# Optimization experiments

Hardware: AMD Instinct MI355X
Metric: run time of the kernel (lower is better)

## Reference

```python
import jax, jax.numpy as jnp
import numpy as np

LOG_2PI = float(np.log(2.0 * np.pi))


def setup_inputs() -> dict:
    key = jax.random.key(0)
    k1, k2, k3 = jax.random.split(key, 3)
    N, D, K = 2_000_000, 16, 32
    data = jax.random.normal(k1, (N, D), dtype=jnp.float32)
    means = jax.random.uniform(k2, (K, D), dtype=jnp.float32)  # torch.rand init
    # torch init is eye expanded per component; perturb slightly so the
    # Cholesky / solve paths are exercised with non-trivial values while
    # A @ A.T stays well-conditioned PD.
    cov_parts = (jnp.eye(D, dtype=jnp.float32)[None, :, :]
                 + 0.1 * jax.random.normal(k3, (K, D, D), dtype=jnp.float32))
    log_weights = jnp.zeros((K,), dtype=jnp.float32)
    return {"data": data, "means": means, "cov_parts": cov_parts,
            "log_weights": log_weights}


def _mixture_loglik(data, means, cov_parts, log_weights):
    D = data.shape[-1]
    # covariance_k = A_k @ A_k^T  -> Cholesky factor L_k (lower)
    cov = jnp.einsum('kij,klj->kil', cov_parts, cov_parts)      # [K, D, D]
    chol = jnp.linalg.cholesky(cov)                             # [K, D, D]

    def comp_logprob(mu, L):
        # MVN log_prob for one component over all N points
        diff = data - mu                                        # [N, D]
        # solve L z = diff^T  -> z: [D, N]
        z = jax.scipy.linalg.solve_triangular(L, diff.T, lower=True)
        quad = jnp.sum(z * z, axis=0)                           # [N]
        logdet = jnp.sum(jnp.log(jnp.diagonal(L)))              # 0.5*logdet(cov)
        return -0.5 * (quad + D * LOG_2PI) - logdet             # [N]

    # [N, K] log-likelihood per point per component
    log_liks = jax.vmap(comp_logprob, in_axes=(0, 0), out_axes=1)(means, chol)
    weighted = log_liks + log_weights ** 2                      # note: squared, per source
    return jnp.mean(jax.nn.logsumexp(weighted, axis=1))


def reference(data, means, cov_parts, log_weights):
    return _mixture_loglik(data, means, cov_parts, log_weights)
```

## Files before the change

### kernel.cpp

```cpp
#include <hip/hip_runtime.h>
#include <math.h>


#define LOG_2PI 1.8378770664093453f
#define INV_LN2 1.4426950408889634f
#define LN2_D   0.6931471805599453

typedef float    float4v __attribute__((ext_vector_type(4)));
typedef float    f32x16  __attribute__((ext_vector_type(16)));
typedef _Float16 f16x8   __attribute__((ext_vector_type(8)));
typedef _Float16 f16x2   __attribute__((ext_vector_type(2)));

union H8 { f16x8 h8; f16x2 h2[4]; };

#if __has_builtin(__builtin_amdgcn_exp2f)
#define EXP2F(x) __builtin_amdgcn_exp2f(x)
#else
#define EXP2F(x) exp2f(x)
#endif
#if __has_builtin(__builtin_amdgcn_logf)
#define LOG2F(x) __builtin_amdgcn_logf(x)
#else
#define LOG2F(x) log2f(x)
#endif

static __device__ __forceinline__ f16x2 pk2(float a, float b) {
#if __has_builtin(__builtin_amdgcn_cvt_pkrtz)
  return __builtin_bit_cast(f16x2, __builtin_amdgcn_cvt_pkrtz(a, b));
#else
  f16x2 r; r[0] = (_Float16)a; r[1] = (_Float16)b; return r;
#endif
}

static __device__ __forceinline__ float partner32(float x, bool lo) {
#if __has_builtin(__builtin_amdgcn_permlane32_swap)
  typedef unsigned u32x2 __attribute__((ext_vector_type(2)));
  unsigned u = __builtin_bit_cast(unsigned, x);
  u32x2 r = __builtin_amdgcn_permlane32_swap(u, u, false, false);
  return __builtin_bit_cast(float, lo ? r[1] : r[0]);
#else
  return __shfl_xor(x, 32, 64);
#endif
}

static __device__ __forceinline__ f16x2 sel2(bool c, f16x2 a, f16x2 b) {
  unsigned ua = __builtin_bit_cast(unsigned, a);
  unsigned ub = __builtin_bit_cast(unsigned, b);
  return __builtin_bit_cast(f16x2, c ? ua : ub);
}

__global__ void setup_kernel(const float* __restrict__ means,
                             const float* __restrict__ cov_parts,
                             const float* __restrict__ log_weights,
                             _Float16* __restrict__ W,
                             unsigned* __restrict__ counter)
{
  const int k = blockIdx.x;
  const int i = threadIdx.x;

  if (k == 0 && i == 0) counter[0] = 0u;

  __shared__ float sA[16][17];
  __shared__ float sC[16][17];
  __shared__ float sMu[16];
  __shared__ float sR[16];

  if (i < 16) {
    #pragma unroll
    for (int j = 0; j < 16; ++j) sA[i][j] = cov_parts[(k*16 + i)*16 + j];
    sMu[i] = means[k*16 + i];
  }
  __syncthreads();

  if (i < 16) {
    #pragma unroll
    for (int j = 0; j < 16; ++j) {
      float acc = 0.f;
      #pragma unroll
      for (int l = 0; l < 16; ++l) acc += sA[i][l] * sA[j][l];
      sC[i][j] = acc;
    }
  }
  __syncthreads();

  for (int j = 0; j < 16; ++j) {
    if (i == j) {
      float d = sC[j][j];
      for (int l = 0; l < j; ++l) d -= sC[j][l]*sC[j][l];
      sC[j][j] = sqrtf(d);
    }
    __syncthreads();
    if (i < 16 && i > j) {
      float a = sC[i][j];
      for (int l = 0; l < j; ++l) a -= sC[i][l]*sC[j][l];
      sC[i][j] = a / sC[j][j];
    }
    __syncthreads();
  }

  if (i < 16) {
    float y[16];
    #pragma unroll
    for (int r = 0; r < 16; ++r) {
      float a = (r == i) ? 1.f : 0.f;
      #pragma unroll
      for (int l = 0; l < r; ++l) a -= sC[r][l] * y[l];
      y[r] = a / sC[r][r];
    }
    #pragma unroll
    for (int r = 0; r < 16; ++r) sA[r][i] = y[r];
  }
  __syncthreads();

  if (i < 16) {
    float p[16];
    #pragma unroll
    for (int j = 0; j < 16; ++j) {
      float acc = 0.f;
      #pragma unroll
      for (int l = 0; l < 16; ++l) acc += sA[l][i] * sA[l][j];
      p[j] = acc;
    }
    float ri = 0.f;
    #pragma unroll
    for (int j = 0; j < 16; ++j) ri += p[j] * sMu[j];
    sR[i] = ri;

    #pragma unroll
    for (int j = 0; j < 16; ++j) {
      W[(size_t)(i*64 + (k + 32*(j >> 3)))*8 + (j & 7)] =
          (_Float16)(-0.5f * INV_LN2 * p[j]);
    }
    W[(size_t)(16*64 + (k + 32*(i >> 3)))*8 + (i & 7)] =
        (_Float16)(INV_LN2 * ri);
  }
  __syncthreads();

  if (i == 0) {
    float logdet = 0.f;
    #pragma unroll
    for (int j = 0; j < 16; ++j) logdet += __logf(sC[j][j]);
    float mupmu = 0.f;
    #pragma unroll
    for (int j = 0; j < 16; ++j) mupmu += sMu[j] * sR[j];
    float lw = log_weights[k];
    float c2v = INV_LN2 * (-0.5f*(mupmu + 16.f*LOG_2PI) - logdet + lw*lw);
    #pragma unroll
    for (int v = 0; v < 8; ++v) {
      W[(size_t)(17*64 + k)*8 + v]      = (v == 0) ? (_Float16)c2v : (_Float16)0.f;
      W[(size_t)(17*64 + k + 32)*8 + v] = (_Float16)0.f;
    }
  }
}

__global__ __launch_bounds__(256, 3) void main_kernel(
    const float* __restrict__ data,
    const _Float16* __restrict__ W,
    float* __restrict__ partials,
    unsigned* __restrict__ counter,
    float* __restrict__ out,
    double scale,
    int ntiles)
{
  const int lane = threadIdx.x & 63;
  const int n32  = lane & 31;
  const bool lo  = lane < 32;
  const int gwave  = (int)((blockIdx.x * blockDim.x + threadIdx.x) >> 6);
  const int nwaves = (int)((gridDim.x * blockDim.x) >> 6);

  f16x8 Wf[18];
  #pragma unroll
  for (int c = 0; c < 18; ++c)
    Wf[c] = *(const f16x8*)(W + (size_t)(c*64 + lane)*8);

  H8 bC;
  #pragma unroll
  for (int j = 0; j < 4; ++j) bC.h2[j] = pk2(0.f, 0.f);
  if (lo) bC.h2[0] = pk2(1.f, 0.f);

  float accsum = 0.f;

  const char* ptrA = (const char*)data + ((size_t)gwave*2048 + (size_t)n32*64);
  const char* ptrB = ptrA + (size_t)nwaves*2048;
  const size_t step2 = (size_t)nwaves * 4096;

  float4v pA0, pA1, pA2, pA3, pB0, pB1, pB2, pB3;
  if (gwave < ntiles) {
    pA0 = *(const float4v*)(ptrA);      pA1 = *(const float4v*)(ptrA + 16);
    pA2 = *(const float4v*)(ptrA + 32); pA3 = *(const float4v*)(ptrA + 48);
  }
  if (gwave + nwaves < ntiles) {
    pB0 = *(const float4v*)(ptrB);      pB1 = *(const float4v*)(ptrB + 16);
    pB2 = *(const float4v*)(ptrB + 32); pB3 = *(const float4v*)(ptrB + 48);
  }

  auto body = [&](float4v& q0, float4v& q1, float4v& q2, float4v& q3,
                  const char*& qptr, int t) {
    f16x2 xh[8];
    xh[0] = pk2(q0[0], q0[1]); xh[1] = pk2(q0[2], q0[3]);
    xh[2] = pk2(q1[0], q1[1]); xh[3] = pk2(q1[2], q1[3]);
    xh[4] = pk2(q2[0], q2[1]); xh[5] = pk2(q2[2], q2[3]);
    xh[6] = pk2(q3[0], q3[1]); xh[7] = pk2(q3[2], q3[3]);

    qptr += step2;
    if (t + 2*nwaves < ntiles) {
      q0 = *(const float4v*)(qptr);      q1 = *(const float4v*)(qptr + 16);
      q2 = *(const float4v*)(qptr + 32); q3 = *(const float4v*)(qptr + 48);
    }

    f16x2 xs[4];
    #pragma unroll
    for (int j = 0; j < 4; ++j) xs[j] = sel2(lo, xh[j], xh[4+j]);

    f32x16 acc;
    #pragma unroll
    for (int r = 0; r < 16; ++r) acc[r] = 0.f;

    #pragma unroll
    for (int c = 0; c < 16; ++c) {
      _Float16 xi = xh[c >> 1][c & 1];
      H8 b;
      #pragma unroll
      for (int j = 0; j < 4; ++j) b.h2[j] = xs[j] * xi;
      acc = __builtin_amdgcn_mfma_f32_32x32x16_f16(Wf[c], b.h8, acc, 0, 0, 0);
    }
    {
      H8 b;
      #pragma unroll
      for (int j = 0; j < 4; ++j) b.h2[j] = xs[j];
      acc = __builtin_amdgcn_mfma_f32_32x32x16_f16(Wf[16], b.h8, acc, 0, 0, 0);
    }
    acc = __builtin_amdgcn_mfma_f32_32x32x16_f16(Wf[17], bC.h8, acc, 0, 0, 0);

    float m = acc[0];
    #pragma unroll
    for (int r = 1; r < 16; ++r) m = fmaxf(m, acc[r]);
    m = fmaxf(m, partner32(m, lo));
    float s = 0.f;
    #pragma unroll
    for (int r = 0; r < 16; ++r) s += EXP2F(acc[r] - m);
    s += partner32(s, lo);
    accsum += m + LOG2F(s);
  };

  if (gwave < ntiles) {
    int t = gwave;
    for (;;) {
      body(pA0, pA1, pA2, pA3, ptrA, t);
      t += nwaves; if (t >= ntiles) break;
      body(pB0, pB1, pB2, pB3, ptrB, t);
      t += nwaves; if (t >= ntiles) break;
    }
  }

  #pragma unroll
  for (int off = 1; off <= 32; off <<= 1)
    accsum += __shfl_xor(accsum, off, 64);

  __shared__ float wsum[4];
  __shared__ int isLast;
  const int wid = (int)(threadIdx.x >> 6);
  if ((threadIdx.x & 63) == 0) wsum[wid] = accsum;
  __syncthreads();
  if (threadIdx.x == 0) {
    partials[blockIdx.x] = wsum[0] + wsum[1] + wsum[2] + wsum[3];
    __threadfence();
    unsigned old = atomicAdd(counter, 1u);
    isLast = (old == gridDim.x - 1) ? 1 : 0;
  }
  __syncthreads();

  if (isLast) {
    __threadfence();
    __shared__ double sd[256];
    double a = 0.0;
    for (int idx = (int)threadIdx.x; idx < (int)gridDim.x; idx += 256)
      a += (double)partials[idx];
    sd[threadIdx.x] = a;
    __syncthreads();
    for (int s = 128; s > 0; s >>= 1) {
      if ((int)threadIdx.x < s) sd[threadIdx.x] += sd[threadIdx.x + s];
      __syncthreads();
    }
    if (threadIdx.x == 0) out[0] = (float)(sd[0] * scale);
  }
}

extern "C" void kernel_launch(void* const* d_in, const int* in_sizes, int n_in,
                              void* d_out, int out_size, void* d_ws, size_t ws_size,
                              hipStream_t stream)
{
  const float* data        = (const float*)d_in[0];
  const float* means       = (const float*)d_in[1];
  const float* cov_parts   = (const float*)d_in[2];
  const float* log_weights = (const float*)d_in[3];

  const int npts   = in_sizes[0] / 16;
  const int ntiles = npts / 32;

  _Float16* W        = (_Float16*)d_ws;
  float*    partials = (float*)((char*)d_ws + 18432);
  unsigned* counter  = (unsigned*)((char*)d_ws + 18432 + 3072);

  const int GRID = 768, BLOCK = 256;
  setup_kernel<<<32, 64, 0, stream>>>(means, cov_parts, log_weights, W, counter);
  main_kernel<<<GRID, BLOCK, 0, stream>>>(data, W, partials, counter,
                                          (float*)d_out,
                                          LN2_D / (2.0 * (double)npts), ntiles);
}
```

Before: 234.4 us.

## Stage data tiles through per-wave LDS with coalesced loads and split accumulators

Global loads now use a coalesced layout: each lane loads 16 contiguous bytes, so every wave covers one tile with two fully contiguous 1 KB accesses. The data is written into a swizzled, double-buffered LDS region per wave and read back in the per-point row layout the MFMA needs. The MFMA chain is also split into two independent accumulators to shorten the dependency chain. The grid shrinks to 512 blocks with launch bounds of 2, which lowers occupancy. In exchange it adds LDS traffic and relies on the ordering of LDS accesses within a wave with no barrier.

Result: faster. 210.1 us (-10.3%).

```diff
diff --git a/kernel.cpp b/kernel.cpp
--- a/kernel.cpp
+++ b/kernel.cpp
@@ -153,7 +153,7 @@
   }
 }
 
-__global__ __launch_bounds__(256, 3) void main_kernel(
+__global__ __launch_bounds__(256, 2) void main_kernel(
     const float* __restrict__ data,
     const _Float16* __restrict__ W,
     float* __restrict__ partials,
@@ -162,11 +162,27 @@
     double scale,
     int ntiles)
 {
-  const int lane = threadIdx.x & 63;
+  const int tid  = (int)threadIdx.x;
+  const int lane = tid & 63;
   const int n32  = lane & 31;
   const bool lo  = lane < 32;
-  const int gwave  = (int)((blockIdx.x * blockDim.x + threadIdx.x) >> 6);
+  const int wid  = tid >> 6;
+  const int gwave  = (int)((blockIdx.x * blockDim.x + tid) >> 6);
   const int nwaves = (int)((gridDim.x * blockDim.x) >> 6);
+
+  __shared__ __align__(16) char lds[4][2][2048];
+  char* Lb0 = &lds[wid][0][0];
+  char* Lb1 = &lds[wid][1][0];
+
+  const int pw0 = lane >> 2, jw = lane & 3;
+  const int pw1 = 16 + pw0;
+  const int wo0 = (pw0*64 + jw*16) ^ ((pw0 & 7) << 4);
+  const int wo1 = (pw1*64 + jw*16) ^ ((pw1 & 7) << 4);
+  const int rx  = (n32 & 7) << 4;
+  const int ro0 = (n32*64 +  0) ^ rx;
+  const int ro1 = (n32*64 + 16) ^ rx;
+  const int ro2 = (n32*64 + 32) ^ rx;
+  const int ro3 = (n32*64 + 48) ^ rx;
 
   f16x8 Wf[18];
   #pragma unroll
@@ -180,41 +196,32 @@
 
   float accsum = 0.f;
 
-  const char* ptrA = (const char*)data + ((size_t)gwave*2048 + (size_t)n32*64);
-  const char* ptrB = ptrA + (size_t)nwaves*2048;
-  const size_t step2 = (size_t)nwaves * 4096;
-
-  float4v pA0, pA1, pA2, pA3, pB0, pB1, pB2, pB3;
-  if (gwave < ntiles) {
-    pA0 = *(const float4v*)(ptrA);      pA1 = *(const float4v*)(ptrA + 16);
-    pA2 = *(const float4v*)(ptrA + 32); pA3 = *(const float4v*)(ptrA + 48);
-  }
-  if (gwave + nwaves < ntiles) {
-    pB0 = *(const float4v*)(ptrB);      pB1 = *(const float4v*)(ptrB + 16);
-    pB2 = *(const float4v*)(ptrB + 32); pB3 = *(const float4v*)(ptrB + 48);
-  }
-
-  auto body = [&](float4v& q0, float4v& q1, float4v& q2, float4v& q3,
-                  const char*& qptr, int t) {
+  const char* base = (const char*)data;
+  auto gload = [&](float4v& a, float4v& b, int t) {
+    const char* p = base + (size_t)t*2048 + (size_t)lane*16;
+    a = *(const float4v*)(p);
+    b = *(const float4v*)(p + 1024);
+  };
+
+  auto compute = [&](const char* Lr) {
+    float4v r0 = *(const float4v*)(Lr + ro0);
+    float4v r1 = *(const float4v*)(Lr + ro1);
+    float4v r2 = *(const float4v*)(Lr + ro2);
+    float4v r3 = *(const float4v*)(Lr + ro3);
+
     f16x2 xh[8];
-    xh[0] = pk2(q0[0], q0[1]); xh[1] = pk2(q0[2], q0[3]);
-    xh[2] = pk2(q1[0], q1[1]); xh[3] = pk2(q1[2], q1[3]);
-    xh[4] = pk2(q2[0], q2[1]); xh[5] = pk2(q2[2], q2[3]);
-    xh[6] = pk2(q3[0], q3[1]); xh[7] = pk2(q3[2], q3[3]);
-
-    qptr += step2;
-    if (t + 2*nwaves < ntiles) {
-      q0 = *(const float4v*)(qptr);      q1 = *(const float4v*)(qptr + 16);
-      q2 = *(const float4v*)(qptr + 32); q3 = *(const float4v*)(qptr + 48);
-    }
+    xh[0] = pk2(r0[0], r0[1]); xh[1] = pk2(r0[2], r0[3]);
+    xh[2] = pk2(r1[0], r1[1]); xh[3] = pk2(r1[2], r1[3]);
+    xh[4] = pk2(r2[0], r2[1]); xh[5] = pk2(r2[2], r2[3]);
+    xh[6] = pk2(r3[0], r3[1]); xh[7] = pk2(r3[2], r3[3]);
 
     f16x2 xs[4];
     #pragma unroll
     for (int j = 0; j < 4; ++j) xs[j] = sel2(lo, xh[j], xh[4+j]);
 
-    f32x16 acc;
-    #pragma unroll
-    for (int r = 0; r < 16; ++r) acc[r] = 0.f;
+    f32x16 acc0, acc1;
+    #pragma unroll
+    for (int r = 0; r < 16; ++r) { acc0[r] = 0.f; acc1[r] = 0.f; }
 
     #pragma unroll
     for (int c = 0; c < 16; ++c) {
@@ -222,15 +229,20 @@
       H8 b;
       #pragma unroll
       for (int j = 0; j < 4; ++j) b.h2[j] = xs[j] * xi;
-      acc = __builtin_amdgcn_mfma_f32_32x32x16_f16(Wf[c], b.h8, acc, 0, 0, 0);
+      if (c & 1)
+        acc1 = __builtin_amdgcn_mfma_f32_32x32x16_f16(Wf[c], b.h8, acc1, 0, 0, 0);
+      else
+        acc0 = __builtin_amdgcn_mfma_f32_32x32x16_f16(Wf[c], b.h8, acc0, 0, 0, 0);
     }
     {
       H8 b;
       #pragma unroll
       for (int j = 0; j < 4; ++j) b.h2[j] = xs[j];
-      acc = __builtin_amdgcn_mfma_f32_32x32x16_f16(Wf[16], b.h8, acc, 0, 0, 0);
-    }
-    acc = __builtin_amdgcn_mfma_f32_32x32x16_f16(Wf[17], bC.h8, acc, 0, 0, 0);
+      acc1 = __builtin_amdgcn_mfma_f32_32x32x16_f16(Wf[16], b.h8, acc1, 0, 0, 0);
+    }
+    acc0 = __builtin_amdgcn_mfma_f32_32x32x16_f16(Wf[17], bC.h8, acc0, 0, 0, 0);
+
+    f32x16 acc = acc0 + acc1;
 
     float m = acc[0];
     #pragma unroll
@@ -243,12 +255,32 @@
     accsum += m + LOG2F(s);
   };
 
-  if (gwave < ntiles) {
-    int t = gwave;
+  float4v A0, A1, B0, B1;
+  const int t0 = gwave;
+  if (t0 < ntiles) gload(A0, A1, t0);
+  if (t0 + nwaves < ntiles) gload(B0, B1, t0 + nwaves);
+  if (t0 < ntiles) {
+    *(float4v*)(Lb0 + wo0) = A0;
+    *(float4v*)(Lb0 + wo1) = A1;
+  }
+
+  if (t0 < ntiles) {
+    int t = t0;
     for (;;) {
-      body(pA0, pA1, pA2, pA3, ptrA, t);
+      if (t + nwaves < ntiles) {
+        *(float4v*)(Lb1 + wo0) = B0;
+        *(float4v*)(Lb1 + wo1) = B1;
+      }
+      if (t + 2*nwaves < ntiles) gload(A0, A1, t + 2*nwaves);
+      compute(Lb0);
       t += nwaves; if (t >= ntiles) break;
-      body(pB0, pB1, pB2, pB3, ptrB, t);
+
+      if (t + nwaves < ntiles) {
+        *(float4v*)(Lb0 + wo0) = A0;
+        *(float4v*)(Lb0 + wo1) = A1;
+      }
+      if (t + 2*nwaves < ntiles) gload(B0, B1, t + 2*nwaves);
+      compute(Lb1);
       t += nwaves; if (t >= ntiles) break;
     }
   }
@@ -259,10 +291,9 @@
 
   __shared__ float wsum[4];
   __shared__ int isLast;
-  const int wid = (int)(threadIdx.x >> 6);
-  if ((threadIdx.x & 63) == 0) wsum[wid] = accsum;
-  __syncthreads();
-  if (threadIdx.x == 0) {
+  if ((tid & 63) == 0) wsum[wid] = accsum;
+  __syncthreads();
+  if (tid == 0) {
     partials[blockIdx.x] = wsum[0] + wsum[1] + wsum[2] + wsum[3];
     __threadfence();
     unsigned old = atomicAdd(counter, 1u);
@@ -274,15 +305,15 @@
     __threadfence();
     __shared__ double sd[256];
     double a = 0.0;
-    for (int idx = (int)threadIdx.x; idx < (int)gridDim.x; idx += 256)
+    for (int idx = tid; idx < (int)gridDim.x; idx += 256)
       a += (double)partials[idx];
-    sd[threadIdx.x] = a;
+    sd[tid] = a;
     __syncthreads();
     for (int s = 128; s > 0; s >>= 1) {
-      if ((int)threadIdx.x < s) sd[threadIdx.x] += sd[threadIdx.x + s];
+      if (tid < s) sd[tid] += sd[tid + s];
       __syncthreads();
     }
-    if (threadIdx.x == 0) out[0] = (float)(sd[0] * scale);
+    if (tid == 0) out[0] = (float)(sd[0] * scale);
   }
 }
 
@@ -302,7 +333,7 @@
   float*    partials = (float*)((char*)d_ws + 18432);
   unsigned* counter  = (unsigned*)((char*)d_ws + 18432 + 3072);
 
-  const int GRID = 768, BLOCK = 256;
+  const int GRID = 512, BLOCK = 256;
   setup_kernel<<<32, 64, 0, stream>>>(means, cov_parts, log_weights, W, counter);
   main_kernel<<<GRID, BLOCK, 0, stream>>>(data, W, partials, counter,
                                           (float*)d_out,
```
